# Kernel tuning notes

Measured on AMD Instinct MI355X. Metric: run time of the kernel, lower is better.

## Reference

```python
import jax, jax.numpy as jnp
import numpy as np
from jax import lax

V_VOX, T_PTS, D, H, W = 12000, 35, 10, 200, 176
EPS = 1e-5


def _bn(x, g, b, axes, shape):
    m = x.mean(axes, keepdims=True)
    v = x.var(axes, keepdims=True)  # biased var, matches torch BN training stats
    return g.reshape(shape) * (x - m) * lax.rsqrt(v + EPS) + b.reshape(shape)


def _conv3d(x, w, b):
    y = lax.conv_general_dilated(x, w, (1, 1, 1), 'SAME',
                                 dimension_numbers=('NCDHW', 'OIDHW', 'NCDHW'))
    return y + b[None, :, None, None, None]


def _conv2d(x, w, b):
    y = lax.conv_general_dilated(x, w, (1, 1), 'SAME',
                                 dimension_numbers=('NCHW', 'OIHW', 'NCHW'))
    return y + b[None, :, None, None]


def setup_inputs() -> dict:
    key = jax.random.key(0)
    ks = jax.random.split(key, 12)
    voxels = jax.random.normal(ks[0], (1, V_VOX, T_PTS, 4), jnp.float32)
    # unique voxel coordinates (the torch loop overwrites on duplicates; unique avoids ambiguity)
    rng = np.random.default_rng(0)
    flat = rng.choice(D * H * W, size=V_VOX, replace=False)
    z = flat // (H * W); rem = flat % (H * W)
    coords = jnp.asarray(np.stack([z, rem // W, rem % W], axis=1), dtype=jnp.int32)
    s = 0.05
    p = dict(
        w_lin=jax.random.normal(ks[1], (32, 4), jnp.float32) * s,
        b_lin=jnp.zeros((32,), jnp.float32),
        g_bn0=jnp.ones((32,), jnp.float32), be_bn0=jnp.zeros((32,), jnp.float32),
        w_c3a=jax.random.normal(ks[2], (64, 32, 3, 3, 3), jnp.float32) * s,
        b_c3a=jnp.zeros((64,), jnp.float32),
        g_bn1=jnp.ones((64,), jnp.float32), be_bn1=jnp.zeros((64,), jnp.float32),
        w_c3b=jax.random.normal(ks[3], (64, 64, 3, 3, 3), jnp.float32) * s,
        b_c3b=jnp.zeros((64,), jnp.float32),
        g_bn2=jnp.ones((64,), jnp.float32), be_bn2=jnp.zeros((64,), jnp.float32),
        w_r1=jax.random.normal(ks[4], (128, 64, 3, 3), jnp.float32) * s,
        b_r1=jnp.zeros((128,), jnp.float32),
        w_r2=jax.random.normal(ks[5], (8, 128, 1, 1), jnp.float32) * s,
        b_r2=jnp.zeros((8,), jnp.float32),
    )
    return dict(voxels=voxels, coords=coords, **p)


def reference(voxels, coords, w_lin, b_lin, g_bn0, be_bn0,
              w_c3a, b_c3a, g_bn1, be_bn1, w_c3b, b_c3b, g_bn2, be_bn2,
              w_r1, b_r1, w_r2, b_r2):
    B, V, T, C = voxels.shape
    # SimpleVFE: linear -> BN1d (batch stats) -> relu -> max over points
    h = voxels.reshape(B * V * T, C) @ w_lin.T + b_lin          # [BVT,32]
    h = jax.nn.relu(_bn(h, g_bn0, be_bn0, 0, (1, 32)))
    feats = h.reshape(B, V, T, 32).max(axis=2)                  # [B,V,32]
    # fused scatter into dense volume (replaces per-voxel python loop)
    volume = jnp.zeros((B, 32, D, H, W), voxels.dtype)
    volume = volume.at[0, :, coords[:, 0], coords[:, 1], coords[:, 2]].set(feats[0])
    # 3D backbone
    x = jax.nn.relu(_bn(_conv3d(volume, w_c3a, b_c3a), g_bn1, be_bn1, (0, 2, 3, 4), (1, 64, 1, 1, 1)))
    x = jax.nn.relu(_bn(_conv3d(x, w_c3b, b_c3b), g_bn2, be_bn2, (0, 2, 3, 4), (1, 64, 1, 1, 1)))
    x = x.mean(axis=2)                                          # collapse depth -> [B,64,H,W]
    # RPN head
    out = _conv2d(jax.nn.relu(_conv2d(x, w_r1, b_r1)), w_r2, b_r2)  # [B,8,H,W]
    box = jnp.concatenate([out[:, 0:3], jnp.exp(out[:, 3:6]),
                           jnp.tanh(out[:, 6:7]), jax.nn.sigmoid(out[:, 7:8])], axis=1)
    return box
```

## Files before the change

kernel.cpp:

```cpp
#include <hip/hip_runtime.h>
#include <math.h>

#define V_VOX 12000
#define T_PTS 35
#define DD 10
#define HH 200
#define WW 176
#define EPSV 1e-5f

#define DP 12
#define HP 202
#define WP 178
#define PPLN (HP * WP)
#define PVOX (DP * PPLN)
#define NPIX (DD * HH * WW)
#define HWPIX (HH * WW)

typedef _Float16 half_t;
typedef _Float16 f16x8 __attribute__((ext_vector_type(8)));
typedef float f32x4 __attribute__((ext_vector_type(4)));

#define WPA_OFF 0
#define WPB_OFF 110592
#define WPR1_OFF 331776
#define STATS_OFF 479232
#define FEATS_OFF 483328
#define VOLP_OFF 2019328
#define X1P_OFF 29633536
#define Y_OFF 84861952
#define PLANE_OFF 129917952
#define R1OUT_OFF 134520320

#define S_BN0S 0
#define S_BN0Q 32
#define S_BN1S 64
#define S_BN1Q 128
#define S_BN2S 192
#define S_BN2Q 256
#define C0A 320
#define C0B 352
#define C1A 384
#define C1B 448
#define C2A 512
#define C2B 576

__device__ __forceinline__ void gload16(const half_t* g, half_t* l) {
    __builtin_amdgcn_global_load_lds(
        (const __attribute__((address_space(1))) void*)g,
        (__attribute__((address_space(3))) void*)l, 16, 0, 0);
}

__global__ void k_pack(const float* __restrict__ w, half_t* __restrict__ wp,
                       int IC, int NT, int OC) {
    int id = blockIdx.x * 256 + threadIdx.x;
    int OCT = OC >> 4, KH = IC >> 5;
    int total = NT * KH * OCT * 512;
    if (id >= total) return;
    int j = id & 7;
    int lane = (id >> 3) & 63;
    int rest = id >> 9;
    int ot = rest % OCT; rest /= OCT;
    int kh = rest % KH;
    int tap = rest / KH;
    int oc = ot * 16 + (lane & 15);
    int ic = kh * 32 + (lane >> 4) * 8 + j;
    wp[id] = (half_t)w[(oc * IC + ic) * NT + tap];
}

__global__ void k_vfe_stats(const float4* __restrict__ vox, const float* __restrict__ w_lin,
                            const float* __restrict__ b_lin, float* __restrict__ S) {
    int tid = blockIdx.x * 256 + threadIdx.x;
    int c = threadIdx.x & 31;
    float4 w = ((const float4*)w_lin)[c];
    float bl = b_lin[c];
    float s = 0.f, q = 0.f;
    const int np = V_VOX * T_PTS;
    int stride = gridDim.x * 8;
    for (int p = tid >> 5; p < np; p += stride) {
        float4 v = vox[p];
        float d = v.x * w.x + v.y * w.y + v.z * w.z + v.w * w.w + bl;
        s += d;
        q += d * d;
    }
    s += __shfl_xor(s, 32);
    q += __shfl_xor(q, 32);
    if ((threadIdx.x & 63) < 32) {
        atomicAdd(&S[S_BN0S + c], s);
        atomicAdd(&S[S_BN0Q + c], q);
    }
}

__global__ void k_bn_final(const float* __restrict__ ss, const float* __restrict__ sq,
                           const float* __restrict__ g, const float* __restrict__ be,
                           float* __restrict__ ca, float* __restrict__ cb, int C, float invN) {
    int c = threadIdx.x;
    if (c >= C) return;
    float m = ss[c] * invN;
    float v = sq[c] * invN - m * m;
    float a = g[c] * rsqrtf(v + EPSV);
    ca[c] = a;
    cb[c] = be[c] - m * a;
}

__global__ void k_vfe_max(const float4* __restrict__ vox, const float* __restrict__ w_lin,
                          const float* __restrict__ b_lin, const float* __restrict__ ca,
                          const float* __restrict__ cb, float* __restrict__ feats) {
    int id = blockIdx.x * 256 + threadIdx.x;
    if (id >= V_VOX * 32) return;
    int c = id & 31;
    int v = id >> 5;
    float4 w = ((const float4*)w_lin)[c];
    float bl = b_lin[c], A = ca[c], B = cb[c];
    float m = 0.f;
    for (int t = 0; t < T_PTS; t++) {
        float4 p = vox[v * T_PTS + t];
        float d = p.x * w.x + p.y * w.y + p.z * w.z + p.w * w.w + bl;
        m = fmaxf(m, A * d + B);
    }
    feats[id] = m;
}

__global__ void k_scatter(const float* __restrict__ feats, const int* __restrict__ coords,
                          half_t* __restrict__ volp) {
    int id = blockIdx.x * 256 + threadIdx.x;
    if (id >= V_VOX * 32) return;
    int c = id & 31;
    int v = id >> 5;
    int z = coords[v * 3 + 0];
    int y = coords[v * 3 + 1];
    int x = coords[v * 3 + 2];
    volp[(((z + 1) * HP + (y + 1)) * WP + (x + 1)) * 32 + c] = (half_t)feats[id];
}

template <int KH, int DZ, int OCTP, bool RELU, bool STATS>
__global__ __launch_bounds__(256, 2) void k_conv(const half_t* __restrict__ in,
                                                 size_t khstride,
                                                 const half_t* __restrict__ wp,
                                                 const float* __restrict__ bias,
                                                 half_t* __restrict__ out,
                                                 float* __restrict__ ssum,
                                                 float* __restrict__ ssq) {
    constexpr int OC = OCTP * 16;
    constexpr int NS = DZ * KH;
    __shared__ __align__(16) half_t tA[2][21 * 512];
    __shared__ __align__(16) half_t tB[2][18 * 512];

    const int tid = threadIdx.x;
    const int lane = tid & 63;
    const int wv = tid >> 6;
    const int x0 = blockIdx.x * 16;
    const int y0b = blockIdx.y * 16;
    const int bz = blockIdx.z;
    const int z0 = (DZ == 3) ? (bz >> 1) : 0;
    const int ocb = (DZ == 3) ? (bz & 1) * 2 : bz * 2;
    const int y0w = y0b + wv * 4;
    const bool valid = (y0w < HH);
    const int colc = lane & 15, grp = lane >> 4;

    unsigned gofsA[6];
#pragma unroll
    for (int i = 0; i < 6; ++i) {
        int run = wv + 4 * i;
        int c = run * 64 + lane;
        if (c > 1295) c = 1295;
        int pixhi = c >> 3, s = c & 7;
        int b = ((s >> 2) ^ (pixhi >> 1)) & 1;
        int q = ((s ^ b) & 1) | ((((s >> 1) ^ pixhi) & 1) << 1);
        int pix = pixhi * 2 + b;
        int row = pix / 18, px = pix - row * 18;
        int srow = y0b + row;
        if (srow > HP - 1) srow = HP - 1;
        gofsA[i] = (unsigned)((srow * WP + x0 + px) * 32 + q * 8);
    }

    f32x4 acc[4][2];
#pragma unroll
    for (int m = 0; m < 4; m++)
#pragma unroll
        for (int n = 0; n < 2; n++) acc[m][n] = (f32x4)(0.f);

    auto STAGE = [&](int s, int buf) {
        const int dz = s / KH, kh = s % KH;
        const half_t* sl = in + (size_t)kh * khstride
                           + (size_t)(z0 + dz) * (DZ == 3 ? (size_t)PPLN * 32 : 0);
#pragma unroll
        for (int i = 0; i < 6; ++i) {
            int run = wv + 4 * i;
            if (run < 21) gload16(sl + gofsA[i], &tA[buf][run * 512]);
        }
#pragma unroll
        for (int i = 0; i < 5; ++i) {
            int r = wv + 4 * i;
            if (r < 18) {
                int tap = r >> 1, hf = r & 1;
                const half_t* g = wp + (((size_t)(dz * 9 + tap) * KH + kh) * OCTP + ocb + hf) * 512
                                  + lane * 8;
                gload16(g, &tB[buf][r * 512]);
            }
        }
    };

    STAGE(0, 0);

#pragma unroll 1
    for (int s = 0; s < NS; ++s) {
        if (s + 1 < NS) {
            STAGE(s + 1, (s + 1) & 1);
            if (wv == 0)      asm volatile("s_waitcnt vmcnt(11)" ::: "memory");
            else if (wv == 1) asm volatile("s_waitcnt vmcnt(10)" ::: "memory");
            else              asm volatile("s_waitcnt vmcnt(9)" ::: "memory");
        } else {
            asm volatile("s_waitcnt vmcnt(0)" ::: "memory");
        }
        __builtin_amdgcn_s_barrier();

        if (valid) {
            const int buf = s & 1;
#pragma unroll
            for (int dx = 0; dx < 3; ++dx) {
                f16x8 Af[6];
#pragma unroll
                for (int r = 0; r < 6; ++r) {
                    int pix = (wv * 4 + r) * 18 + colc + dx;
                    int ah = ((pix << 5) | (grp << 3)) ^ ((pix & 7) << 3);
                    Af[r] = *(const f16x8*)&tA[buf][ah];
                }
#pragma unroll
                for (int dy = 0; dy < 3; ++dy) {
                    f16x8 Bf[2];
#pragma unroll
                    for (int n = 0; n < 2; ++n)
                        Bf[n] = *(const f16x8*)&tB[buf][((dy * 3 + dx) * 2 + n) * 512 + lane * 8];
#pragma unroll
                    for (int m = 0; m < 4; ++m)
#pragma unroll
                        for (int n = 0; n < 2; ++n)
                            acc[m][n] = __builtin_amdgcn_mfma_f32_16x16x32_f16(
                                Af[dy + m], Bf[n], acc[m][n], 0, 0, 0);
                }
            }
        }
        asm volatile("s_waitcnt lgkmcnt(0)" ::: "memory");
        __builtin_amdgcn_s_barrier();
    }

    if (!valid) return;
#pragma unroll
    for (int n = 0; n < 2; ++n) {
        int oc = (ocb + n) * 16 + colc;
        float bv = bias[oc];
        float s = 0.f, q = 0.f;
#pragma unroll
        for (int m = 0; m < 4; ++m) {
            int yy = y0w + m;
#pragma unroll
            for (int i = 0; i < 4; ++i) {
                int xx = x0 + grp * 4 + i;
                float v = acc[m][n][i] + bv;
                if (STATS) { s += v; q += v * v; }
                float w = RELU ? fmaxf(v, 0.f) : v;
                out[((size_t)(z0 * HH + yy) * WW + xx) * OC + oc] = (half_t)w;
            }
        }
        if (STATS) {
            s += __shfl_xor(s, 16); s += __shfl_xor(s, 32);
            q += __shfl_xor(q, 16); q += __shfl_xor(q, 32);
            if (lane < 16) {
                atomicAdd(&ssum[oc], s);
                atomicAdd(&ssq[oc], q);
            }
        }
    }
}

__global__ void k_activate(const half_t* __restrict__ y1, const float* __restrict__ ca,
                           const float* __restrict__ cb, half_t* __restrict__ xp) {
    int id = blockIdx.x * 256 + threadIdx.x;
    if (id >= PVOX * 8) return;
    int c0 = (id & 7) * 8;
    int pix = id >> 3;
    int zp = pix / PPLN;
    int rem = pix - zp * PPLN;
    int yp = rem / WP;
    int xq = rem - yp * WP;
    f16x8 o;
    if (zp >= 1 && zp <= DD && yp >= 1 && yp <= HH && xq >= 1 && xq <= WW) {
        size_t p = ((size_t)((zp - 1) * HH + (yp - 1)) * WW + (xq - 1));
        f16x8 v = *(const f16x8*)(y1 + p * 64 + c0);
#pragma unroll
        for (int j = 0; j < 8; j++)
            o[j] = (half_t)fmaxf(ca[c0 + j] * (float)v[j] + cb[c0 + j], 0.f);
    } else {
#pragma unroll
        for (int j = 0; j < 8; j++) o[j] = (half_t)0.f;
    }
    int khp = c0 >> 5;
    *(f16x8*)(xp + (size_t)khp * PVOX * 32 + (size_t)pix * 32 + (c0 & 31)) = o;
}

__global__ void k_depthmean(const half_t* __restrict__ y2, const float* __restrict__ ca,
                            const float* __restrict__ cb, half_t* __restrict__ plane) {
    int id = blockIdx.x * 256 + threadIdx.x;
    int c = id & 63;
    int pix = id >> 6;
    int yp = pix / WP;
    int xq = pix - yp * WP;
    float val = 0.f;
    if (yp >= 1 && yp <= HH && xq >= 1 && xq <= WW) {
        float A = ca[c], B = cb[c], s = 0.f;
        const half_t* base = y2 + ((size_t)(yp - 1) * WW + (xq - 1)) * 64 + c;
#pragma unroll
        for (int z = 0; z < DD; z++)
            s += fmaxf(A * (float)base[(size_t)z * HWPIX * 64] + B, 0.f);
        val = s * 0.1f;
    }
    int khp = c >> 5;
    plane[(size_t)khp * PPLN * 32 + (size_t)pix * 32 + (c & 31)] = (half_t)val;
}

__global__ void k_r2(const half_t* __restrict__ r1o, const float* __restrict__ w,
                     const float* __restrict__ bias, float* __restrict__ outp) {
    __shared__ float wsm[1024];
    for (int i = threadIdx.x; i < 1024; i += 256) wsm[i] = w[i];
    __syncthreads();
    int p = blockIdx.x * 256 + threadIdx.x;
    if (p >= HWPIX) return;
    float acc[8];
#pragma unroll
    for (int o = 0; o < 8; o++) acc[o] = bias[o];
    const half_t* rb = r1o + (size_t)p * 128;
#pragma unroll 4
    for (int icb = 0; icb < 128; icb += 8) {
        f16x8 v = *(const f16x8*)(rb + icb);
#pragma unroll
        for (int j = 0; j < 8; j++) {
            float vv = (float)v[j];
#pragma unroll
            for (int o = 0; o < 8; o++) acc[o] += vv * wsm[o * 128 + icb + j];
        }
    }
    outp[0 * HWPIX + p] = acc[0];
    outp[1 * HWPIX + p] = acc[1];
    outp[2 * HWPIX + p] = acc[2];
    outp[3 * HWPIX + p] = expf(acc[3]);
    outp[4 * HWPIX + p] = expf(acc[4]);
    outp[5 * HWPIX + p] = expf(acc[5]);
    outp[6 * HWPIX + p] = tanhf(acc[6]);
    outp[7 * HWPIX + p] = 1.f / (1.f + expf(-acc[7]));
}

extern "C" void kernel_launch(void* const* d_in, const int* in_sizes, int n_in,
                              void* d_out, int out_size, void* d_ws, size_t ws_size,
                              hipStream_t stream) {
    const float4* voxels = (const float4*)d_in[0];
    const int* coords = (const int*)d_in[1];
    const float* w_lin = (const float*)d_in[2];
    const float* b_lin = (const float*)d_in[3];
    const float* g_bn0 = (const float*)d_in[4];
    const float* be_bn0 = (const float*)d_in[5];
    const float* w_c3a = (const float*)d_in[6];
    const float* b_c3a = (const float*)d_in[7];
    const float* g_bn1 = (const float*)d_in[8];
    const float* be_bn1 = (const float*)d_in[9];
    const float* w_c3b = (const float*)d_in[10];
    const float* b_c3b = (const float*)d_in[11];
    const float* g_bn2 = (const float*)d_in[12];
    const float* be_bn2 = (const float*)d_in[13];
    const float* w_r1 = (const float*)d_in[14];
    const float* b_r1 = (const float*)d_in[15];
    const float* w_r2 = (const float*)d_in[16];
    const float* b_r2 = (const float*)d_in[17];

    char* ws = (char*)d_ws;
    half_t* wpA = (half_t*)(ws + WPA_OFF);
    half_t* wpB = (half_t*)(ws + WPB_OFF);
    half_t* wpR1 = (half_t*)(ws + WPR1_OFF);
    float* S = (float*)(ws + STATS_OFF);
    float* feats = (float*)(ws + FEATS_OFF);
    half_t* volp = (half_t*)(ws + VOLP_OFF);
    half_t* x1p = (half_t*)(ws + X1P_OFF);
    half_t* Y = (half_t*)(ws + Y_OFF);
    half_t* plane = (half_t*)(ws + PLANE_OFF);
    half_t* r1out = (half_t*)(ws + R1OUT_OFF);
    float* outp = (float*)d_out;

    hipMemsetAsync(S, 0, 320 * sizeof(float), stream);
    hipMemsetAsync(volp, 0, (size_t)PVOX * 32 * sizeof(half_t), stream);

    k_pack<<<216, 256, 0, stream>>>(w_c3a, wpA, 32, 27, 64);
    k_pack<<<432, 256, 0, stream>>>(w_c3b, wpB, 64, 27, 64);
    k_pack<<<288, 256, 0, stream>>>(w_r1, wpR1, 64, 9, 128);

    k_vfe_stats<<<512, 256, 0, stream>>>(voxels, w_lin, b_lin, S);
    k_bn_final<<<1, 64, 0, stream>>>(S + S_BN0S, S + S_BN0Q, g_bn0, be_bn0,
                                     S + C0A, S + C0B, 32, 1.f / 420000.f);
    k_vfe_max<<<1500, 256, 0, stream>>>(voxels, w_lin, b_lin, S + C0A, S + C0B, feats);
    k_scatter<<<1500, 256, 0, stream>>>(feats, coords, volp);

    k_conv<1, 3, 4, false, true><<<dim3(11, 13, 20), 256, 0, stream>>>(
        volp, 0, wpA, b_c3a, Y, S + S_BN1S, S + S_BN1Q);
    k_bn_final<<<1, 64, 0, stream>>>(S + S_BN1S, S + S_BN1Q, g_bn1, be_bn1,
                                     S + C1A, S + C1B, 64, 1.f / 352000.f);
    k_activate<<<13484, 256, 0, stream>>>(Y, S + C1A, S + C1B, x1p);

    k_conv<2, 3, 4, false, true><<<dim3(11, 13, 20), 256, 0, stream>>>(
        x1p, (size_t)PVOX * 32, wpB, b_c3b, Y, S + S_BN2S, S + S_BN2Q);
    k_bn_final<<<1, 64, 0, stream>>>(S + S_BN2S, S + S_BN2Q, g_bn2, be_bn2,
                                     S + C2A, S + C2B, 64, 1.f / 352000.f);

    k_depthmean<<<8989, 256, 0, stream>>>(Y, S + C2A, S + C2B, plane);

    k_conv<2, 1, 8, true, false><<<dim3(11, 13, 4), 256, 0, stream>>>(
        plane, (size_t)PPLN * 32, wpR1, b_r1, r1out, nullptr, nullptr);
    k_r2<<<138, 256, 0, stream>>>(r1out, w_r2, b_r2, outp);
}
```

Measured before the change: 464.5 us.

## Load conv weights directly into registers and drop LDS weight staging

```diff
diff --git a/kernel.cpp b/kernel.cpp
--- a/kernel.cpp
+++ b/kernel.cpp
@@ -133,7 +133,7 @@
 }
 
 template <int KH, int DZ, int OCTP, bool RELU, bool STATS>
-__global__ __launch_bounds__(256, 2) void k_conv(const half_t* __restrict__ in,
+__global__ __launch_bounds__(256, 3) void k_conv(const half_t* __restrict__ in,
                                                  size_t khstride,
                                                  const half_t* __restrict__ wp,
                                                  const float* __restrict__ bias,
@@ -142,8 +142,7 @@
                                                  float* __restrict__ ssq) {
     constexpr int OC = OCTP * 16;
     constexpr int NS = DZ * KH;
-    __shared__ __align__(16) half_t tA[2][21 * 512];
-    __shared__ __align__(16) half_t tB[2][18 * 512];
+    __shared__ __align__(16) half_t tA[2][24 * 512];
 
     const int tid = threadIdx.x;
     const int lane = tid & 63;
@@ -179,36 +178,33 @@
 #pragma unroll
         for (int n = 0; n < 2; n++) acc[m][n] = (f32x4)(0.f);
 
-    auto STAGE = [&](int s, int buf) {
+    auto STAGEA = [&](int s, int buf) {
         const int dz = s / KH, kh = s % KH;
         const half_t* sl = in + (size_t)kh * khstride
                            + (size_t)(z0 + dz) * (DZ == 3 ? (size_t)PPLN * 32 : 0);
 #pragma unroll
         for (int i = 0; i < 6; ++i) {
             int run = wv + 4 * i;
-            if (run < 21) gload16(sl + gofsA[i], &tA[buf][run * 512]);
-        }
-#pragma unroll
-        for (int i = 0; i < 5; ++i) {
-            int r = wv + 4 * i;
-            if (r < 18) {
-                int tap = r >> 1, hf = r & 1;
-                const half_t* g = wp + (((size_t)(dz * 9 + tap) * KH + kh) * OCTP + ocb + hf) * 512
-                                  + lane * 8;
-                gload16(g, &tB[buf][r * 512]);
-            }
+            gload16(sl + gofsA[i], &tA[buf][run * 512]);
         }
     };
 
-    STAGE(0, 0);
+    STAGEA(0, 0);
 
 #pragma unroll 1
     for (int s = 0; s < NS; ++s) {
+        const int dz = s / KH, kh = s % KH;
+        f16x8 Breg[9][2];
+#pragma unroll
+        for (int tap = 0; tap < 9; ++tap)
+#pragma unroll
+            for (int n = 0; n < 2; ++n)
+                Breg[tap][n] = *(const f16x8*)(wp
+                    + (((size_t)(dz * 9 + tap) * KH + kh) * OCTP + ocb + n) * 512 + lane * 8);
+        asm volatile("" ::: "memory");
         if (s + 1 < NS) {
-            STAGE(s + 1, (s + 1) & 1);
-            if (wv == 0)      asm volatile("s_waitcnt vmcnt(11)" ::: "memory");
-            else if (wv == 1) asm volatile("s_waitcnt vmcnt(10)" ::: "memory");
-            else              asm volatile("s_waitcnt vmcnt(9)" ::: "memory");
+            STAGEA(s + 1, (s + 1) & 1);
+            asm volatile("s_waitcnt vmcnt(6)" ::: "memory");
         } else {
             asm volatile("s_waitcnt vmcnt(0)" ::: "memory");
         }
@@ -226,18 +222,13 @@
                     Af[r] = *(const f16x8*)&tA[buf][ah];
                 }
 #pragma unroll
-                for (int dy = 0; dy < 3; ++dy) {
-                    f16x8 Bf[2];
-#pragma unroll
-                    for (int n = 0; n < 2; ++n)
-                        Bf[n] = *(const f16x8*)&tB[buf][((dy * 3 + dx) * 2 + n) * 512 + lane * 8];
+                for (int dy = 0; dy < 3; ++dy)
 #pragma unroll
                     for (int m = 0; m < 4; ++m)
 #pragma unroll
                         for (int n = 0; n < 2; ++n)
                             acc[m][n] = __builtin_amdgcn_mfma_f32_16x16x32_f16(
-                                Af[dy + m], Bf[n], acc[m][n], 0, 0, 0);
-                }
+                                Af[dy + m], Breg[dy * 3 + dx][n], acc[m][n], 0, 0, 0);
             }
         }
         asm volatile("s_waitcnt lgkmcnt(0)" ::: "memory");
```

Result: no change. 461.7 us (-0.6%).
